# Kernel optimization log

Measured on AMD Instinct MI355X. Metric: run time of the kernel, lower is better.

## Reference

```python
import jax, jax.numpy as jnp
import numpy as np

# Problem dims
N_LIG, N_PROT = 10000, 40000
N = N_LIG + N_PROT            # total nodes in batched graph
E = 400000                    # total edges (avg degree 8)
B = 512                       # number of pocket graphs in batch
F_LIG, F_PROT = 74, 1280      # ligand / protein node feature dims
H, D = 4, 64                  # GAT heads, per-head dim
HD = H * D                    # hidden size == PROJ_DIM == 256


def setup_inputs() -> dict:
    key = jax.random.key(0)
    ks = jax.random.split(key, 16)
    s = jnp.float32(0.05)  # keep activations tame
    return {
        "ligand_x":  jax.random.normal(ks[0], (N_LIG, F_LIG), jnp.float32),
        "protein_x": jax.random.normal(ks[1], (N_PROT, F_PROT), jnp.float32),
        "W_lig":  jax.random.normal(ks[2], (F_LIG, HD), jnp.float32) * s,
        "W_prot": jax.random.normal(ks[3], (F_PROT, HD), jnp.float32) * s,
        "W1":     jax.random.normal(ks[4], (HD, HD), jnp.float32) * s,
        "a1_src": jax.random.normal(ks[5], (H, D), jnp.float32) * s,
        "a1_dst": jax.random.normal(ks[6], (H, D), jnp.float32) * s,
        "W2":     jax.random.normal(ks[7], (HD, HD), jnp.float32) * s,
        "a2_src": jax.random.normal(ks[8], (H, D), jnp.float32) * s,
        "a2_dst": jax.random.normal(ks[9], (H, D), jnp.float32) * s,
        "W_out":  jax.random.normal(ks[10], (HD + 1, 1), jnp.float32) * s,
        "b_out":  jnp.zeros((1,), jnp.float32),
        "edge_src":  jax.random.randint(ks[11], (E,), 0, N, jnp.int32),
        "edge_dst":  jax.random.randint(ks[12], (E,), 0, N, jnp.int32),
        "graph_ids": jnp.sort(jax.random.randint(ks[13], (N,), 0, B, jnp.int32)),
        "scores":    jax.random.uniform(ks[14], (B, 1), jnp.float32),
    }


def _gat_layer(x, W, a_src, a_dst, src, dst):
    """Multi-head GAT layer over an edge list. x:[N,HD] -> [N,HD]."""
    n = x.shape[0]
    h = (x @ W).reshape(n, H, D)                               # [N,H,D]
    att_s = jnp.einsum('nhd,hd->nh', h, a_src)                 # [N,H]
    att_d = jnp.einsum('nhd,hd->nh', h, a_dst)
    e = jax.nn.leaky_relu(att_s[src] + att_d[dst], 0.2)        # [E,H]
    # edge softmax over incoming edges of each destination node
    m = jax.ops.segment_max(e, dst, num_segments=n)            # [N,H]
    w = jnp.exp(e - m[dst])                                    # [E,H]
    denom = jax.ops.segment_sum(w, dst, num_segments=n)        # [N,H]
    agg = jax.ops.segment_sum(h[src] * w[..., None], dst, num_segments=n)  # [N,H,D]
    out = agg / (denom[..., None] + 1e-9)
    return jax.nn.elu(out).reshape(n, HD)


def reference(ligand_x, protein_x, W_lig, W_prot, W1, a1_src, a1_dst,
              W2, a2_src, a2_dst, W_out, b_out,
              edge_src, edge_dst, graph_ids, scores):
    # per-node-type input projection into shared hidden space
    x = jnp.concatenate([ligand_x @ W_lig, protein_x @ W_prot], axis=0)  # [N,HD]
    h = _gat_layer(x, W1, a1_src, a1_dst, edge_src, edge_dst)
    h = _gat_layer(h, W2, a2_src, a2_dst, edge_src, edge_dst)
    # mean pooling per graph -> [B, PROJ_DIM]
    gsum = jax.ops.segment_sum(h, graph_ids, num_segments=B)
    cnt = jax.ops.segment_sum(jnp.ones((h.shape[0], 1), h.dtype), graph_ids, num_segments=B)
    pooled = gsum / jnp.maximum(cnt, 1.0)
    # concat docking score, final linear (dropout is identity at eval)
    feat = jnp.concatenate([pooled, scores], axis=1)           # [B, PROJ_DIM+1]
    return feat @ W_out + b_out                                 # [B,1]
```

## Files before the change

kernel.cpp:

```cpp
#include <hip/hip_runtime.h>
#include <hip/hip_bf16.h>

#define N_LIG   10000
#define N_PROT  40000
#define NN      50000
#define EDGES   400000
#define BATCH   512
#define F_LIG   74
#define F_PROT  1280
#define HD      256
#define HEADS   4
#define DIM     64

typedef __bf16 bf16x8 __attribute__((ext_vector_type(8)));
typedef __bf16 bf16x4 __attribute__((ext_vector_type(4)));
typedef float  f32x4  __attribute__((ext_vector_type(4)));


__global__ void k_hist(const int* __restrict__ dst, int* __restrict__ counts, int E) {
    int e = blockIdx.x * blockDim.x + threadIdx.x;
    if (e < E) atomicAdd(&counts[dst[e]], 1);
}

__global__ __launch_bounds__(1024) void k_scan1(const int* __restrict__ counts,
                                                int* __restrict__ incl,
                                                int* __restrict__ bsum, int N) {
    __shared__ int tmp[1024];
    int i = blockIdx.x * 1024 + threadIdx.x;
    int v = (i < N) ? counts[i] : 0;
    tmp[threadIdx.x] = v;
    __syncthreads();
    for (int off = 1; off < 1024; off <<= 1) {
        int add = (threadIdx.x >= (unsigned)off) ? tmp[threadIdx.x - off] : 0;
        __syncthreads();
        tmp[threadIdx.x] += add;
        __syncthreads();
    }
    if (i < N) incl[i] = tmp[threadIdx.x];
    if (threadIdx.x == 1023) bsum[blockIdx.x] = tmp[1023];
}

__global__ void k_scan2(int* __restrict__ bsum, int nb, int* __restrict__ row_ptr, int N, int E) {
    if (threadIdx.x == 0 && blockIdx.x == 0) {
        int run = 0;
        for (int i = 0; i < nb; ++i) { int v = bsum[i]; bsum[i] = run; run += v; }
        row_ptr[N] = E;
    }
}

__global__ __launch_bounds__(1024) void k_scan3(const int* __restrict__ incl,
                                                const int* __restrict__ counts,
                                                const int* __restrict__ bsum,
                                                int* __restrict__ row_ptr, int N) {
    int i = blockIdx.x * 1024 + threadIdx.x;
    if (i < N) row_ptr[i] = bsum[blockIdx.x] + incl[i] - counts[i];
}

__global__ void k_scatter(const int* __restrict__ src, const int* __restrict__ dst,
                          const int* __restrict__ row_ptr, int* __restrict__ cursor,
                          int* __restrict__ csr_src, int E) {
    int e = blockIdx.x * blockDim.x + threadIdx.x;
    if (e < E) {
        int d = dst[e];
        int pos = row_ptr[d] + atomicAdd(&cursor[d], 1);
        csr_src[pos] = src[e];
    }
}

__global__ __launch_bounds__(256) void k_wcvt(const float* __restrict__ W,
                                              __bf16* __restrict__ Bt, int K, int Kp) {
    int n = blockIdx.x;
    for (int k = threadIdx.x; k < Kp; k += blockDim.x)
        Bt[(size_t)n * Kp + k] = (k < K) ? (__bf16)W[(size_t)k * HD + n] : (__bf16)0.f;
}

__global__ __launch_bounds__(128) void k_apad(const float* __restrict__ A, float* __restrict__ Ap) {
    int row = blockIdx.x, t = threadIdx.x;
    if (t < 96) Ap[(size_t)row * 96 + t] = (t < F_LIG) ? A[(size_t)row * F_LIG + t] : 0.f;
}

__device__ __forceinline__ void gload16(const void* g, void* l) {
    __builtin_amdgcn_global_load_lds(
        (const __attribute__((address_space(1))) void*)g,
        (__attribute__((address_space(3))) void*)l, 16, 0, 0);
}

__device__ __forceinline__ int xcd_swz(int orig, int nwg) {
    int q = nwg >> 3, r = nwg & 7;
    int xcd = orig & 7, idx = orig >> 3;
    return (xcd < r ? xcd * (q + 1) : r * (q + 1) + (xcd - r) * q) + idx;
}

template <int MODE>
__global__ __launch_bounds__(256, 3)
void mfma_gemm(const float* __restrict__ A, const __bf16* __restrict__ Bt,
               float* __restrict__ C,
               __bf16* __restrict__ Hbf, float* __restrict__ atts, float* __restrict__ attd,
               const float* __restrict__ a_src, const float* __restrict__ a_dst,
               int M, int K, int Kp, int nwg) {
    __shared__ __align__(16) unsigned char smem[49152];
    float*  sA = (float*)smem;
    __bf16* sB = (__bf16*)(smem + 24576);

    int wg   = xcd_swz(blockIdx.x, nwg);
    int tid  = threadIdx.x;
    int bm   = (wg >> 1) * 64;
    int bn   = (wg & 1) * 128;
    int lane = tid & 63, wave = tid >> 6;
    int wr   = wave >> 1, wc = wave & 1;
    int l15  = lane & 15, quad = lane >> 4;

    f32x4 acc[2][4];
    #pragma unroll
    for (int i = 0; i < 2; ++i)
        #pragma unroll
        for (int j = 0; j < 4; ++j)
            acc[i][j] = (f32x4){0.f, 0.f, 0.f, 0.f};

    int caA = wave * 2;
    int rlA = lane >> 3, csA = (lane & 7) ^ rlA;
    int rlB = lane >> 2, csB = (lane & 3) ^ (rlB & 3);

    int gmA[2];
    const __bf16* gB[2];
    #pragma unroll
    for (int it = 0; it < 2; ++it) {
        int gm = bm + (caA + it) * 8 + rlA;
        gmA[it] = (gm < M) ? gm : (M - 1);
        gB[it] = Bt + (size_t)(bn + (caA + it) * 16 + rlB) * Kp + csB * 8;
    }

    auto stage = [&](int buf, int k0) {
        #pragma unroll
        for (int it = 0; it < 2; ++it)
            gload16(A + (size_t)gmA[it] * K + k0 + csA * 4,
                    sA + buf * 2048 + (caA + it) * 256);
        #pragma unroll
        for (int it = 0; it < 2; ++it)
            gload16(gB[it] + k0,
                    sB + buf * 4096 + (caA + it) * 512);
    };

    int nsteps = K >> 5;

    stage(0, 0);
    if (nsteps > 1) {
        stage(1, 32);
        asm volatile("s_waitcnt vmcnt(4)" ::: "memory");
    } else {
        asm volatile("s_waitcnt vmcnt(0)" ::: "memory");
    }
    __builtin_amdgcn_s_barrier();
    __builtin_amdgcn_sched_barrier(0);

    int cur = 0, stg = 2;
    for (int s = 0; s < nsteps; ++s) {
        if (s + 2 < nsteps) stage(stg, (s + 2) * 32);

        bf16x8 bfr[4];
        #pragma unroll
        for (int j = 0; j < 4; ++j) {
            int rowb = wc * 64 + j * 16 + l15;
            int ch = quad ^ (l15 & 3);
            bfr[j] = *(const bf16x8*)&sB[cur * 4096 + rowb * 32 + ch * 8];
        }
        bf16x8 af[2], al[2];
        #pragma unroll
        for (int i = 0; i < 2; ++i) {
            int rowa = wr * 32 + i * 16 + l15;
            int ch0 = (quad * 2)     ^ (l15 & 7);
            int ch1 = (quad * 2 + 1) ^ (l15 & 7);
            f32x4 p0 = *(const f32x4*)&sA[cur * 2048 + rowa * 32 + ch0 * 4];
            f32x4 p1 = *(const f32x4*)&sA[cur * 2048 + rowa * 32 + ch1 * 4];
            #pragma unroll
            for (int c = 0; c < 8; ++c) {
                float x = (c < 4) ? p0[c] : p1[c - 4];
                __bf16 h = (__bf16)x;
                af[i][c] = h;
                if (MODE) al[i][c] = (__bf16)(x - (float)h);
            }
        }

        #pragma unroll
        for (int i = 0; i < 2; ++i)
            #pragma unroll
            for (int j = 0; j < 4; ++j) {
                acc[i][j] = __builtin_amdgcn_mfma_f32_16x16x32_bf16(af[i], bfr[j], acc[i][j], 0, 0, 0);
                if (MODE)
                    acc[i][j] = __builtin_amdgcn_mfma_f32_16x16x32_bf16(al[i], bfr[j], acc[i][j], 0, 0, 0);
            }

        asm volatile("s_waitcnt lgkmcnt(0)" ::: "memory");
        __builtin_amdgcn_sched_barrier(0);
        if (s + 2 < nsteps)      asm volatile("s_waitcnt vmcnt(4)" ::: "memory");
        else if (s + 1 < nsteps) asm volatile("s_waitcnt vmcnt(0)" ::: "memory");
        __builtin_amdgcn_s_barrier();
        __builtin_amdgcn_sched_barrier(0);

        cur = (cur == 2) ? 0 : cur + 1;
        stg = (stg == 2) ? 0 : stg + 1;
    }

    if (MODE == 0) {
        #pragma unroll
        for (int i = 0; i < 2; ++i)
            #pragma unroll
            for (int r = 0; r < 4; ++r) {
                int m = bm + wr * 32 + i * 16 + quad * 4 + r;
                if (m < M) {
                    #pragma unroll
                    for (int j = 0; j < 4; ++j)
                        C[(size_t)m * HD + bn + wc * 64 + j * 16 + l15] = acc[i][j][r];
                }
            }
    } else {
        int head = (bn >> 6) + wc;
        float as[4], ad2[4];
        #pragma unroll
        for (int j = 0; j < 4; ++j) {
            as[j]  = a_src[head * DIM + j * 16 + l15];
            ad2[j] = a_dst[head * DIM + j * 16 + l15];
        }
        #pragma unroll
        for (int i = 0; i < 2; ++i)
            #pragma unroll
            for (int r = 0; r < 4; ++r) {
                int m = bm + wr * 32 + i * 16 + quad * 4 + r;
                bool ok = m < M;
                float s = 0.f, t = 0.f;
                #pragma unroll
                for (int j = 0; j < 4; ++j) {
                    float v = acc[i][j][r];
                    if (ok) Hbf[(size_t)m * HD + head * DIM + j * 16 + l15] = (__bf16)v;
                    s += v * as[j];
                    t += v * ad2[j];
                }
                #pragma unroll
                for (int mask = 1; mask <= 8; mask <<= 1) {
                    s += __shfl_xor(s, mask, 64);
                    t += __shfl_xor(t, mask, 64);
                }
                if (ok && l15 == 0) {
                    atts[m * HEADS + head] = s;
                    attd[m * HEADS + head] = t;
                }
            }
    }
}

__global__ __launch_bounds__(256) void gat_agg(const __bf16* __restrict__ hW,
                                               const float* __restrict__ att_s,
                                               const float* __restrict__ att_d,
                                               const int* __restrict__ row_ptr,
                                               const int* __restrict__ csr_src,
                                               float* __restrict__ out, int N) {
    int n = blockIdx.x;
    int t = threadIdx.x;
    int lane = t & 63, head = t >> 6;
    int r0 = row_ptr[n], deg = row_ptr[n + 1] - r0;
    float ad = att_d[n * HEADS + head];

    float m = -INFINITY;
    for (int base = 0; base < deg; base += 64) {
        int i = base + lane;
        float e = -INFINITY;
        if (i < deg) {
            int s = csr_src[r0 + i];
            float x = att_s[s * HEADS + head] + ad;
            e = (x >= 0.f) ? x : 0.2f * x;
        }
        for (int off = 32; off > 0; off >>= 1) e = fmaxf(e, __shfl_xor(e, off, 64));
        m = fmaxf(m, e);
    }

    f32x4 acc4 = (f32x4){0.f, 0.f, 0.f, 0.f};
    float wsum = 0.f;
    int sub = lane >> 4;
    int dq  = lane & 15;
    for (int base = 0; base < deg; base += 64) {
        int i = base + lane;
        float w = 0.f; int s = 0;
        if (i < deg) {
            s = csr_src[r0 + i];
            float x = att_s[s * HEADS + head] + ad;
            x = (x >= 0.f) ? x : 0.2f * x;
            w = expf(x - m);
        }
        wsum += w;
        int cnt = min(64, deg - base);
        for (int j0 = 0; j0 < cnt; j0 += 8) {
            #pragma unroll
            for (int g = 0; g < 2; ++g) {
                int e0 = j0 + g * 4 + sub;
                int ec = min(e0, cnt - 1);
                int   sj = __shfl(s, ec, 64);
                float wj = __shfl(w, ec, 64);
                if (e0 >= cnt) wj = 0.f;
                bf16x4 v4 = *(const bf16x4*)&hW[(size_t)sj * HD + head * DIM + dq * 4];
                #pragma unroll
                for (int c = 0; c < 4; ++c) acc4[c] += wj * (float)v4[c];
            }
        }
    }
    #pragma unroll
    for (int c = 0; c < 4; ++c) {
        acc4[c] += __shfl_xor(acc4[c], 16, 64);
        acc4[c] += __shfl_xor(acc4[c], 32, 64);
    }
    for (int off = 32; off > 0; off >>= 1) wsum += __shfl_xor(wsum, off, 64);
    if (sub == 0) {
        float inv = 1.f / (wsum + 1e-9f);
        f32x4 o;
        #pragma unroll
        for (int c = 0; c < 4; ++c) {
            float v = acc4[c] * inv;
            o[c] = (v > 0.f) ? v : expm1f(v);
        }
        *(f32x4*)&out[(size_t)n * HD + head * DIM + dq * 4] = o;
    }
}

__global__ __launch_bounds__(256) void pool_out(const float* __restrict__ h,
                                                const int* __restrict__ gid,
                                                const float* __restrict__ W_out,
                                                const float* __restrict__ b_out,
                                                const float* __restrict__ scores,
                                                float* __restrict__ out, int N) {
    int b = blockIdx.x;
    int j = threadIdx.x;
    int l = 0, r = N;
    while (l < r) { int mid = (l + r) >> 1; if (gid[mid] < b) l = mid + 1; else r = mid; }
    int lo = l;
    r = N;
    while (l < r) { int mid = (l + r) >> 1; if (gid[mid] < b + 1) l = mid + 1; else r = mid; }
    int hi = l;

    float sum = 0.f;
    for (int n = lo; n < hi; ++n) sum += h[(size_t)n * HD + j];
    int cnt = hi - lo;
    float pooled = sum / fmaxf((float)cnt, 1.f);
    float val = pooled * W_out[j];

    __shared__ float red[256];
    red[j] = val;
    __syncthreads();
    for (int s = 128; s > 0; s >>= 1) {
        if (j < s) red[j] += red[j + s];
        __syncthreads();
    }
    if (j == 0) {
        out[b] = red[0] + scores[b] * W_out[HD] + b_out[0];
    }
}


static inline size_t al256(size_t x) { return (x + 255) & ~(size_t)255; }

#define KP_LIG  96
#define KP_PROT 1280
#define KP_HID  256

extern "C" void kernel_launch(void* const* d_in, const int* in_sizes, int n_in,
                              void* d_out, int out_size, void* d_ws, size_t ws_size,
                              hipStream_t stream) {
    const float* ligand_x  = (const float*)d_in[0];
    const float* protein_x = (const float*)d_in[1];
    const float* W_lig     = (const float*)d_in[2];
    const float* W_prot    = (const float*)d_in[3];
    const float* W1        = (const float*)d_in[4];
    const float* a1_src    = (const float*)d_in[5];
    const float* a1_dst    = (const float*)d_in[6];
    const float* W2        = (const float*)d_in[7];
    const float* a2_src    = (const float*)d_in[8];
    const float* a2_dst    = (const float*)d_in[9];
    const float* W_out     = (const float*)d_in[10];
    const float* b_out     = (const float*)d_in[11];
    const int*   edge_src  = (const int*)d_in[12];
    const int*   edge_dst  = (const int*)d_in[13];
    const int*   graph_ids = (const int*)d_in[14];
    const float* scores    = (const float*)d_in[15];
    float* out = (float*)d_out;

    char* w = (char*)d_ws;
    float*  xbuf = (float*)w;           w += al256((size_t)NN * HD * 4);
    __bf16* Hbf  = (__bf16*)w;          w += al256((size_t)NN * HD * 2);
    float* atts = (float*)w;            w += al256((size_t)NN * HEADS * 4);
    float* attd = (float*)w;            w += al256((size_t)NN * HEADS * 4);
    int* counts  = (int*)w;             w += al256((size_t)NN * 4);
    int* incl    = (int*)w;             w += al256((size_t)NN * 4);
    int* bsum    = (int*)w;             w += al256(64 * 4);
    int* row_ptr = (int*)w;             w += al256((size_t)(NN + 1) * 4);
    int* cursor  = (int*)w;             w += al256((size_t)NN * 4);
    int* csr_src = (int*)w;             w += al256((size_t)EDGES * 4);
    __bf16* Bt_lig  = (__bf16*)w;       w += al256((size_t)HD * KP_LIG * 2);
    __bf16* Bt_prot = (__bf16*)w;       w += al256((size_t)HD * KP_PROT * 2);
    __bf16* Bt_W1   = (__bf16*)w;       w += al256((size_t)HD * KP_HID * 2);
    __bf16* Bt_W2   = (__bf16*)w;       w += al256((size_t)HD * KP_HID * 2);
    float* Apad     = (float*)w;        w += al256((size_t)N_LIG * KP_LIG * 4);

    const int NB_SCAN = (NN + 1023) / 1024;

    hipMemsetAsync(counts, 0, (size_t)NN * 4, stream);
    hipMemsetAsync(cursor, 0, (size_t)NN * 4, stream);

    k_wcvt<<<HD, 256, 0, stream>>>(W_lig,  Bt_lig,  F_LIG,  KP_LIG);
    k_wcvt<<<HD, 256, 0, stream>>>(W_prot, Bt_prot, F_PROT, KP_PROT);
    k_wcvt<<<HD, 256, 0, stream>>>(W1,     Bt_W1,   HD,     KP_HID);
    k_wcvt<<<HD, 256, 0, stream>>>(W2,     Bt_W2,   HD,     KP_HID);
    k_apad<<<N_LIG, 128, 0, stream>>>(ligand_x, Apad);

    k_hist<<<(EDGES + 255) / 256, 256, 0, stream>>>(edge_dst, counts, EDGES);
    k_scan1<<<NB_SCAN, 1024, 0, stream>>>(counts, incl, bsum, NN);
    k_scan2<<<1, 1, 0, stream>>>(bsum, NB_SCAN, row_ptr, NN, EDGES);
    k_scan3<<<NB_SCAN, 1024, 0, stream>>>(incl, counts, bsum, row_ptr, NN);
    k_scatter<<<(EDGES + 255) / 256, 256, 0, stream>>>(edge_src, edge_dst, row_ptr,
                                                       cursor, csr_src, EDGES);

    {
        int nwg = 2 * ((N_LIG + 63) / 64);
        mfma_gemm<0><<<nwg, 256, 0, stream>>>(
            Apad, Bt_lig, xbuf, nullptr, nullptr, nullptr, nullptr, nullptr,
            N_LIG, KP_LIG, KP_LIG, nwg);
    }
    {
        int nwg = 2 * ((N_PROT + 63) / 64);
        mfma_gemm<0><<<nwg, 256, 0, stream>>>(
            protein_x, Bt_prot, xbuf + (size_t)N_LIG * HD, nullptr, nullptr, nullptr,
            nullptr, nullptr, N_PROT, KP_PROT, KP_PROT, nwg);
    }

    {
        int nwg = 2 * ((NN + 63) / 64);
        mfma_gemm<1><<<nwg, 256, 0, stream>>>(
            xbuf, Bt_W1, nullptr, Hbf, atts, attd, a1_src, a1_dst, NN, KP_HID, KP_HID, nwg);
    }
    gat_agg<<<NN, 256, 0, stream>>>(Hbf, atts, attd, row_ptr, csr_src, xbuf, NN);

    {
        int nwg = 2 * ((NN + 63) / 64);
        mfma_gemm<1><<<nwg, 256, 0, stream>>>(
            xbuf, Bt_W2, nullptr, Hbf, atts, attd, a2_src, a2_dst, NN, KP_HID, KP_HID, nwg);
    }
    gat_agg<<<NN, 256, 0, stream>>>(Hbf, atts, attd, row_ptr, csr_src, xbuf, NN);

    pool_out<<<BATCH, 256, 0, stream>>>(xbuf, graph_ids, W_out, b_out, scores, out, NN);
}
```

Baseline: 726.5 us.

## Replace LDS-staged projection GEMM with register double-buffered direct-load MFMA kernel

Adds a new projection GEMM that loads A (fp32) and B (bf16) straight from global memory into registers, converts A to bf16 in registers, and software-pipelines two k-steps so loads overlap MFMAs, with no LDS staging or barriers. The ligand input padding is widened to 128 columns so K is a multiple of the 64-wide double step. The aim is to remove LDS round-trips and sync overhead in the memory-bound protein projection (40000x1280 fp32 input). In exchange, global loads are less coalesced, since each lane reads 32 bytes from a different row, and register pressure is higher.

Measured after the change: 845.4 us. +16.4%, slower.

```diff
diff --git a/kernel.cpp b/kernel.cpp
--- a/kernel.cpp
+++ b/kernel.cpp
@@ -76,7 +76,7 @@
 
 __global__ __launch_bounds__(128) void k_apad(const float* __restrict__ A, float* __restrict__ Ap) {
     int row = blockIdx.x, t = threadIdx.x;
-    if (t < 96) Ap[(size_t)row * 96 + t] = (t < F_LIG) ? A[(size_t)row * F_LIG + t] : 0.f;
+    Ap[(size_t)row * 128 + t] = (t < F_LIG) ? A[(size_t)row * F_LIG + t] : 0.f;
 }
 
 __device__ __forceinline__ void gload16(const void* g, void* l) {
@@ -89,6 +89,92 @@
     int q = nwg >> 3, r = nwg & 7;
     int xcd = orig & 7, idx = orig >> 3;
     return (xcd < r ? xcd * (q + 1) : r * (q + 1) + (xcd - r) * q) + idx;
+}
+
+__global__ __launch_bounds__(256, 4)
+void gemm_proj(const float* __restrict__ A, const __bf16* __restrict__ Bt,
+               float* __restrict__ C, int M, int K, int nwg) {
+    int wg   = xcd_swz(blockIdx.x, nwg);
+    int tid  = threadIdx.x;
+    int bm   = (wg >> 1) * 64;
+    int bn   = (wg & 1) * 128;
+    int lane = tid & 63, wave = tid >> 6;
+    int wr   = wave >> 1, wc = wave & 1;
+    int l15  = lane & 15, quad = lane >> 4;
+
+    f32x4 acc[2][4];
+    #pragma unroll
+    for (int i = 0; i < 2; ++i)
+        #pragma unroll
+        for (int j = 0; j < 4; ++j)
+            acc[i][j] = (f32x4){0.f, 0.f, 0.f, 0.f};
+
+    int aoff[2];
+    #pragma unroll
+    for (int i = 0; i < 2; ++i) {
+        int r = bm + wr * 32 + i * 16 + l15;
+        if (r >= M) r = M - 1;
+        aoff[i] = r * K + quad * 8;
+    }
+    int boff[4];
+    #pragma unroll
+    for (int j = 0; j < 4; ++j)
+        boff[j] = (bn + wc * 64 + j * 16 + l15) * K + quad * 8;
+
+    int nsteps = K >> 5;
+    int kmax   = K - 32;
+
+    f32x4  arA[2][2], arB[2][2];
+    bf16x8 acv0[2], acv1[2];
+    bf16x8 bf0[4], bf1[4];
+
+#define LOADA(dst, k0) { int kk = (k0); \
+    _Pragma("unroll") for (int i = 0; i < 2; ++i) { \
+        dst[i][0] = *(const f32x4*)(A + aoff[i] + kk); \
+        dst[i][1] = *(const f32x4*)(A + aoff[i] + kk + 4); } }
+#define LOADB(dst, k0) { int kk = (k0); \
+    _Pragma("unroll") for (int j = 0; j < 4; ++j) \
+        dst[j] = *(const bf16x8*)(Bt + boff[j] + kk); }
+#define CVT(d, s) { \
+    _Pragma("unroll") for (int i = 0; i < 2; ++i) \
+        _Pragma("unroll") for (int c = 0; c < 8; ++c) \
+            d[i][c] = (__bf16)((c < 4) ? s[i][0][c] : s[i][1][c - 4]); }
+#define MFMA8(a, b) { \
+    _Pragma("unroll") for (int i = 0; i < 2; ++i) \
+        _Pragma("unroll") for (int j = 0; j < 4; ++j) \
+            acc[i][j] = __builtin_amdgcn_mfma_f32_16x16x32_bf16(a[i], b[j], acc[i][j], 0, 0, 0); }
+
+    LOADA(arB, 0);
+    LOADA(arA, min(32, kmax));
+    LOADB(bf0, 0);
+    CVT(acv0, arB);
+
+    for (int s = 0; s < nsteps; s += 2) {
+        LOADA(arB, min((s + 2) * 32, kmax));
+        LOADB(bf1, min((s + 1) * 32, kmax));
+        MFMA8(acv0, bf0);
+        CVT(acv1, arA);
+        LOADA(arA, min((s + 3) * 32, kmax));
+        LOADB(bf0, min((s + 2) * 32, kmax));
+        MFMA8(acv1, bf1);
+        CVT(acv0, arB);
+    }
+#undef LOADA
+#undef LOADB
+#undef CVT
+#undef MFMA8
+
+    #pragma unroll
+    for (int i = 0; i < 2; ++i)
+        #pragma unroll
+        for (int r = 0; r < 4; ++r) {
+            int m = bm + wr * 32 + i * 16 + quad * 4 + r;
+            if (m < M) {
+                #pragma unroll
+                for (int j = 0; j < 4; ++j)
+                    C[(size_t)m * HD + bn + wc * 64 + j * 16 + l15] = acc[i][j][r];
+            }
+        }
 }
 
 template <int MODE>
@@ -356,7 +442,7 @@
 
 static inline size_t al256(size_t x) { return (x + 255) & ~(size_t)255; }
 
-#define KP_LIG  96
+#define KP_LIG  128
 #define KP_PROT 1280
 #define KP_HID  256
 
@@ -418,15 +504,12 @@
 
     {
         int nwg = 2 * ((N_LIG + 63) / 64);
-        mfma_gemm<0><<<nwg, 256, 0, stream>>>(
-            Apad, Bt_lig, xbuf, nullptr, nullptr, nullptr, nullptr, nullptr,
-            N_LIG, KP_LIG, KP_LIG, nwg);
+        gemm_proj<<<nwg, 256, 0, stream>>>(Apad, Bt_lig, xbuf, N_LIG, KP_LIG, nwg);
     }
     {
         int nwg = 2 * ((N_PROT + 63) / 64);
-        mfma_gemm<0><<<nwg, 256, 0, stream>>>(
-            protein_x, Bt_prot, xbuf + (size_t)N_LIG * HD, nullptr, nullptr, nullptr,
-            nullptr, nullptr, N_PROT, KP_PROT, KP_PROT, nwg);
+        gemm_proj<<<nwg, 256, 0, stream>>>(protein_x, Bt_prot, xbuf + (size_t)N_LIG * HD,
+                                           N_PROT, KP_PROT, nwg);
     }
 
     {
```

## Assign one wavefront per destination node covering all heads in GAT aggregation

Applied to the files above, without the earlier changes.

The GAT aggregation kernel now maps each 64-lane wavefront to one destination node and handles all four heads in it, instead of one block per node with one wave per head. Edge indices and the four attention logits are loaded once per edge as vector loads and shared across heads. A fast path for degree at most 64 computes the softmax max and weights in a single pass, skipping the second gather over edges. The cost is more registers per thread for four head accumulators, and four times fewer blocks launched.

Result: faster. 668.7 us (-7.9%).

```diff
diff --git a/kernel.cpp b/kernel.cpp
--- a/kernel.cpp
+++ b/kernel.cpp
@@ -254,69 +254,130 @@
                                                const int* __restrict__ row_ptr,
                                                const int* __restrict__ csr_src,
                                                float* __restrict__ out, int N) {
-    int n = blockIdx.x;
-    int t = threadIdx.x;
-    int lane = t & 63, head = t >> 6;
+    int n = blockIdx.x * 4 + (threadIdx.x >> 6);
+    if (n >= N) return;
+    int lane = threadIdx.x & 63;
+    int sub  = lane >> 4;
+    int dq   = lane & 15;
     int r0 = row_ptr[n], deg = row_ptr[n + 1] - r0;
-    float ad = att_d[n * HEADS + head];
-
-    float m = -INFINITY;
-    for (int base = 0; base < deg; base += 64) {
-        int i = base + lane;
-        float e = -INFINITY;
-        if (i < deg) {
-            int s = csr_src[r0 + i];
-            float x = att_s[s * HEADS + head] + ad;
-            e = (x >= 0.f) ? x : 0.2f * x;
-        }
-        for (int off = 32; off > 0; off >>= 1) e = fmaxf(e, __shfl_xor(e, off, 64));
-        m = fmaxf(m, e);
-    }
-
-    f32x4 acc4 = (f32x4){0.f, 0.f, 0.f, 0.f};
-    float wsum = 0.f;
-    int sub = lane >> 4;
-    int dq  = lane & 15;
-    for (int base = 0; base < deg; base += 64) {
-        int i = base + lane;
-        float w = 0.f; int s = 0;
-        if (i < deg) {
-            s = csr_src[r0 + i];
-            float x = att_s[s * HEADS + head] + ad;
-            x = (x >= 0.f) ? x : 0.2f * x;
-            w = expf(x - m);
-        }
-        wsum += w;
-        int cnt = min(64, deg - base);
-        for (int j0 = 0; j0 < cnt; j0 += 8) {
-            #pragma unroll
-            for (int g = 0; g < 2; ++g) {
-                int e0 = j0 + g * 4 + sub;
-                int ec = min(e0, cnt - 1);
-                int   sj = __shfl(s, ec, 64);
-                float wj = __shfl(w, ec, 64);
-                if (e0 >= cnt) wj = 0.f;
-                bf16x4 v4 = *(const bf16x4*)&hW[(size_t)sj * HD + head * DIM + dq * 4];
+    f32x4 ad4 = *(const f32x4*)&att_d[n * HEADS];
+
+    f32x4 acc[4];
+    #pragma unroll
+    for (int h = 0; h < HEADS; ++h) acc[h] = (f32x4){0.f, 0.f, 0.f, 0.f};
+    f32x4 wsum4 = (f32x4){0.f, 0.f, 0.f, 0.f};
+
+    if (deg <= 64) {
+        bool act = lane < deg;
+        int sj = act ? csr_src[r0 + lane] : 0;
+        f32x4 a4 = act ? *(const f32x4*)&att_s[sj * HEADS] : (f32x4){0.f, 0.f, 0.f, 0.f};
+        f32x4 x4;
+        #pragma unroll
+        for (int h = 0; h < HEADS; ++h) {
+            float v = a4[h] + ad4[h];
+            v = (v >= 0.f) ? v : 0.2f * v;
+            x4[h] = act ? v : -INFINITY;
+        }
+        f32x4 m4 = x4;
+        for (int off = 32; off > 0; off >>= 1)
+            #pragma unroll
+            for (int h = 0; h < HEADS; ++h)
+                m4[h] = fmaxf(m4[h], __shfl_xor(m4[h], off, 64));
+        f32x4 w4;
+        #pragma unroll
+        for (int h = 0; h < HEADS; ++h)
+            w4[h] = act ? expf(x4[h] - m4[h]) : 0.f;
+        wsum4 = w4;
+
+        for (int g0 = 0; g0 < deg; g0 += 4) {
+            int e  = g0 + sub;
+            int ec = min(e, deg - 1);
+            int se = __shfl(sj, ec, 64);
+            bool eact = e < deg;
+            #pragma unroll
+            for (int h = 0; h < HEADS; ++h) {
+                float wh = __shfl(w4[h], ec, 64);
+                if (!eact) wh = 0.f;
+                bf16x4 v = *(const bf16x4*)&hW[(size_t)se * HD + h * DIM + dq * 4];
                 #pragma unroll
-                for (int c = 0; c < 4; ++c) acc4[c] += wj * (float)v4[c];
-            }
-        }
-    }
+                for (int c = 0; c < 4; ++c) acc[h][c] += wh * (float)v[c];
+            }
+        }
+    } else {
+        f32x4 m4 = (f32x4){-INFINITY, -INFINITY, -INFINITY, -INFINITY};
+        for (int base = 0; base < deg; base += 64) {
+            int i = base + lane;
+            bool act = i < deg;
+            int sj = act ? csr_src[r0 + i] : 0;
+            f32x4 a4 = act ? *(const f32x4*)&att_s[sj * HEADS] : (f32x4){0.f, 0.f, 0.f, 0.f};
+            #pragma unroll
+            for (int h = 0; h < HEADS; ++h) {
+                float v = a4[h] + ad4[h];
+                v = (v >= 0.f) ? v : 0.2f * v;
+                m4[h] = fmaxf(m4[h], act ? v : -INFINITY);
+            }
+        }
+        for (int off = 32; off > 0; off >>= 1)
+            #pragma unroll
+            for (int h = 0; h < HEADS; ++h)
+                m4[h] = fmaxf(m4[h], __shfl_xor(m4[h], off, 64));
+
+        for (int base = 0; base < deg; base += 64) {
+            int i = base + lane;
+            bool act = i < deg;
+            int sj = act ? csr_src[r0 + i] : 0;
+            f32x4 a4 = act ? *(const f32x4*)&att_s[sj * HEADS] : (f32x4){0.f, 0.f, 0.f, 0.f};
+            f32x4 w4;
+            #pragma unroll
+            for (int h = 0; h < HEADS; ++h) {
+                float v = a4[h] + ad4[h];
+                v = (v >= 0.f) ? v : 0.2f * v;
+                w4[h] = act ? expf(v - m4[h]) : 0.f;
+            }
+            #pragma unroll
+            for (int h = 0; h < HEADS; ++h) wsum4[h] += w4[h];
+            int cnt = min(64, deg - base);
+            for (int g0 = 0; g0 < cnt; g0 += 4) {
+                int e  = g0 + sub;
+                int ec = min(e, cnt - 1);
+                int se = __shfl(sj, ec, 64);
+                bool eact = e < cnt;
+                #pragma unroll
+                for (int h = 0; h < HEADS; ++h) {
+                    float wh = __shfl(w4[h], ec, 64);
+                    if (!eact) wh = 0.f;
+                    bf16x4 v = *(const bf16x4*)&hW[(size_t)se * HD + h * DIM + dq * 4];
+                    #pragma unroll
+                    for (int c = 0; c < 4; ++c) acc[h][c] += wh * (float)v[c];
+                }
+            }
+        }
+    }
+
     #pragma unroll
-    for (int c = 0; c < 4; ++c) {
-        acc4[c] += __shfl_xor(acc4[c], 16, 64);
-        acc4[c] += __shfl_xor(acc4[c], 32, 64);
-    }
-    for (int off = 32; off > 0; off >>= 1) wsum += __shfl_xor(wsum, off, 64);
+    for (int h = 0; h < HEADS; ++h)
+        #pragma unroll
+        for (int c = 0; c < 4; ++c) {
+            acc[h][c] += __shfl_xor(acc[h][c], 16, 64);
+            acc[h][c] += __shfl_xor(acc[h][c], 32, 64);
+        }
+    for (int off = 32; off > 0; off >>= 1)
+        #pragma unroll
+        for (int h = 0; h < HEADS; ++h)
+            wsum4[h] += __shfl_xor(wsum4[h], off, 64);
+
     if (sub == 0) {
-        float inv = 1.f / (wsum + 1e-9f);
-        f32x4 o;
-        #pragma unroll
-        for (int c = 0; c < 4; ++c) {
-            float v = acc4[c] * inv;
-            o[c] = (v > 0.f) ? v : expm1f(v);
-        }
-        *(f32x4*)&out[(size_t)n * HD + head * DIM + dq * 4] = o;
+        #pragma unroll
+        for (int h = 0; h < HEADS; ++h) {
+            float inv = 1.f / (wsum4[h] + 1e-9f);
+            f32x4 o;
+            #pragma unroll
+            for (int c = 0; c < 4; ++c) {
+                float v = acc[h][c] * inv;
+                o[c] = (v > 0.f) ? v : expm1f(v);
+            }
+            *(f32x4*)&out[(size_t)n * HD + h * DIM + dq * 4] = o;
+        }
     }
 }
 
@@ -434,14 +495,14 @@
         mfma_gemm<1><<<nwg, 256, 0, stream>>>(
             xbuf, Bt_W1, nullptr, Hbf, atts, attd, a1_src, a1_dst, NN, KP_HID, KP_HID, nwg);
     }
-    gat_agg<<<NN, 256, 0, stream>>>(Hbf, atts, attd, row_ptr, csr_src, xbuf, NN);
+    gat_agg<<<(NN + 3) / 4, 256, 0, stream>>>(Hbf, atts, attd, row_ptr, csr_src, xbuf, NN);
 
     {
         int nwg = 2 * ((NN + 63) / 64);
         mfma_gemm<1><<<nwg, 256, 0, stream>>>(
             xbuf, Bt_W2, nullptr, Hbf, atts, attd, a2_src, a2_dst, NN, KP_HID, KP_HID, nwg);
     }
-    gat_agg<<<NN, 256, 0, stream>>>(Hbf, atts, attd, row_ptr, csr_src, xbuf, NN);
+    gat_agg<<<(NN + 3) / 4, 256, 0, stream>>>(Hbf, atts, attd, row_ptr, csr_src, xbuf, NN);
 
     pool_out<<<BATCH, 256, 0, stream>>>(xbuf, graph_ids, W_out, b_out, scores, out, NN);
 }
```
